# Performance work log

Measured on AMD Instinct MI355X. Metric: run time of the kernel, lower is better.

## Reference

```python
import jax, jax.numpy as jnp
import numpy as np

B, CITY, H, E, IN = 512, 100, 256, 256, 2
D2 = 2 * H  # num_directions * hidden_size
PEN = 1e6   # already_played_penalty


def _cell(x, h, c, Wih, Whh, b):
    # PyTorch LSTM cell, gate order i,f,g,o
    g = x @ Wih.T + h @ Whh.T + b
    i, f, gg, o = jnp.split(g, 4, axis=-1)
    c = jax.nn.sigmoid(f) * c + jax.nn.sigmoid(i) * jnp.tanh(gg)
    h = jax.nn.sigmoid(o) * jnp.tanh(c)
    return h, c


def _run_lstm(xs, Wih, Whh, b, reverse):
    # xs: [B, T, E] -> outputs [B, T, H], final (h, c)
    Bsz, hdim = xs.shape[0], Whh.shape[1]
    init = (jnp.zeros((Bsz, hdim), xs.dtype), jnp.zeros((Bsz, hdim), xs.dtype))
    def step(carry, x):
        h, c = _cell(x, carry[0], carry[1], Wih, Whh, b)
        return (h, c), h
    (h, c), hs = jax.lax.scan(step, init, jnp.swapaxes(xs, 0, 1), reverse=reverse)
    return jnp.swapaxes(hs, 0, 1), h, c


def setup_inputs() -> dict:
    key = jax.random.key(0)
    ks = iter(jax.random.split(key, 32))
    nrm = lambda shape: 0.1 * jax.random.normal(next(ks), shape, dtype=jnp.float32)
    return {
        "inputs": jax.random.normal(next(ks), (B, CITY, IN), dtype=jnp.float32),
        "test_roads": jax.random.randint(next(ks), (B, CITY), 0, CITY, dtype=jnp.int32),
        "W_embed": nrm((E, IN)),
        "enc_Wih_f": nrm((4 * H, E)), "enc_Whh_f": nrm((4 * H, H)), "enc_b_f": nrm((4 * H,)),
        "enc_Wih_b": nrm((4 * H, E)), "enc_Whh_b": nrm((4 * H, H)), "enc_b_b": nrm((4 * H,)),
        "dec_Wih_f": nrm((4 * H, D2)), "dec_Whh_f": nrm((4 * H, H)), "dec_b_f": nrm((4 * H,)),
        "dec_Wih_b": nrm((4 * H, D2)), "dec_Whh_b": nrm((4 * H, H)), "dec_b_b": nrm((4 * H,)),
        "W_ref": nrm((D2, D2)), "W_q": nrm((D2, D2)), "v": nrm((D2,)),
        "W_ref2": nrm((D2, D2)), "W_q2": nrm((D2, D2)), "v2": nrm((D2,)),
    }


def _forward(inputs, test_roads, W_embed,
             enc_Wih_f, enc_Whh_f, enc_b_f, enc_Wih_b, enc_Whh_b, enc_b_b,
             dec_Wih_f, dec_Whh_f, dec_b_f, dec_Wih_b, dec_Whh_b, dec_b_b,
             W_ref, W_q, v, W_ref2, W_q2, v2):
    Bsz, city, _ = inputs.shape
    emb = inputs @ W_embed.T                                  # [B, city, E]
    enc_f, hf0, cf0 = _run_lstm(emb, enc_Wih_f, enc_Whh_f, enc_b_f, False)
    enc_b, hb0, cb0 = _run_lstm(emb, enc_Wih_b, enc_Whh_b, enc_b_b, True)
    Enc = jnp.concatenate([enc_f, enc_b], axis=-1)            # [B, city, D2]
    # dropout p=0 -> Enc is loop-invariant; hoist the two ref projections
    ref1 = Enc @ W_ref.T                                      # [B, city, D2]
    ref2 = Enc @ W_ref2.T                                     # [B, city, D2]

    def step(carry, tgt):
        x, hf, cf, hb, cb, played, loss = carry
        hf, cf = _cell(x, hf, cf, dec_Wih_f, dec_Whh_f, dec_b_f)
        hb, cb = _cell(x, hb, cb, dec_Wih_b, dec_Whh_b, dec_b_b)
        dec_out = jnp.concatenate([hf, hb], axis=-1)          # [B, D2]
        ow = jnp.tanh(ref1 + (dec_out @ W_q.T)[:, None, :]) @ v - PEN * played   # [B, city]
        aw = jax.nn.softmax(jnp.tanh(ref2 + (x @ W_q2.T)[:, None, :]) @ v2, axis=1)
        sel = jnp.argmax(ow, axis=1)                          # [B]
        x_new = jnp.einsum('bj,bjk->bk', aw, Enc)             # [B, D2]
        played = played + jax.nn.one_hot(sel, city, dtype=played.dtype)
        ce = jax.nn.logsumexp(ow, axis=1) - jnp.take_along_axis(ow, tgt[:, None], axis=1)[:, 0]
        return (x_new, hf, cf, hb, cb, played, loss + ce), None

    x0 = jnp.zeros((Bsz, Enc.shape[-1]), inputs.dtype)
    played0 = jnp.zeros((Bsz, city), inputs.dtype)
    loss0 = jnp.zeros((Bsz,), inputs.dtype)
    carry, _ = jax.lax.scan(step, (x0, hf0, cf0, hb0, cb0, played0, loss0),
                            test_roads.T.astype(jnp.int32))
    return carry[-1]                                          # path_loss [B]


def reference(inputs, test_roads, W_embed,
              enc_Wih_f, enc_Whh_f, enc_b_f, enc_Wih_b, enc_Whh_b, enc_b_b,
              dec_Wih_f, dec_Whh_f, dec_b_f, dec_Wih_b, dec_Whh_b, dec_b_b,
              W_ref, W_q, v, W_ref2, W_q2, v2):
    return _forward(inputs, test_roads, W_embed,
                    enc_Wih_f, enc_Whh_f, enc_b_f, enc_Wih_b, enc_Whh_b, enc_b_b,
                    dec_Wih_f, dec_Whh_f, dec_b_f, dec_Wih_b, dec_Whh_b, dec_b_b,
                    W_ref, W_q, v, W_ref2, W_q2, v2)
```

## Files before the change

### kernel.cpp

```cpp
#include <hip/hip_runtime.h>
#include <hip/hip_fp16.h>
#include <math.h>

namespace {
constexpr int Bn  = 512;
constexpr int Tn  = 100;
constexpr int Hn  = 256;
constexpr int En  = 256;
constexpr int D2n = 512;
constexpr int G4n = 1024;
constexpr float PENf = 1e6f;
constexpr size_t BIGN = (size_t)Bn * Tn * D2n;
constexpr int FLAG_STRIDE = 32;
constexpr int DBLK = 896;
constexpr size_t BAR_UINTS = (256 + DBLK) * FLAG_STRIDE + 64;
}

using short8  = __attribute__((ext_vector_type(8))) short;
using us8     = __attribute__((ext_vector_type(8))) unsigned short;
using floatx4 = __attribute__((ext_vector_type(4))) float;

template<typename T> __device__ __forceinline__ float cvt_to_f(T x);
template<> __device__ __forceinline__ float cvt_to_f<float>(float x) { return x; }
template<> __device__ __forceinline__ float cvt_to_f<__half>(__half x) {
  return __half2float(x);
}
template<typename T> __device__ __forceinline__ T cvt_from_f(float x);
template<> __device__ __forceinline__ float cvt_from_f<float>(float x) { return x; }
template<> __device__ __forceinline__ __half cvt_from_f<__half>(float x) {
  return __float2half(x);
}
__device__ __forceinline__ float h2f_bits(unsigned short b) {
  __half_raw r; r.x = b; return __half2float(__half(r));
}
__device__ __forceinline__ float fast_exp(float x) {
  return __builtin_amdgcn_exp2f(x * 1.44269504088896340736f);
}
__device__ __forceinline__ float sigmoidf(float x) {
  return __builtin_amdgcn_rcpf(1.0f + fast_exp(-x));
}
__device__ __forceinline__ float fast_tanhf(float x) {
  return 1.0f - 2.0f * __builtin_amdgcn_rcpf(fast_exp(2.0f * x) + 1.0f);
}

__device__ __forceinline__ float loadf_dev(const float* p) {
  return __uint_as_float(__hip_atomic_load((const unsigned*)p, __ATOMIC_RELAXED,
                                           __HIP_MEMORY_SCOPE_AGENT));
}
__device__ __forceinline__ void storef_dev(float* p, float v) {
  __hip_atomic_store((unsigned*)p, __float_as_uint(v), __ATOMIC_RELAXED,
                     __HIP_MEMORY_SCOPE_AGENT);
}
__device__ __forceinline__ float4 load4_dev(const float* p) {
  const unsigned long long a = __hip_atomic_load((const unsigned long long*)p,
      __ATOMIC_RELAXED, __HIP_MEMORY_SCOPE_AGENT);
  const unsigned long long b = __hip_atomic_load((const unsigned long long*)p + 1,
      __ATOMIC_RELAXED, __HIP_MEMORY_SCOPE_AGENT);
  float4 r;
  r.x = __uint_as_float((unsigned)a);  r.y = __uint_as_float((unsigned)(a >> 32));
  r.z = __uint_as_float((unsigned)b);  r.w = __uint_as_float((unsigned)(b >> 32));
  return r;
}
__device__ __forceinline__ void store2_dev(float* p, const float2 v) {
  const unsigned long long a = (unsigned long long)__float_as_uint(v.x) |
                               ((unsigned long long)__float_as_uint(v.y) << 32);
  __hip_atomic_store((unsigned long long*)p, a, __ATOMIC_RELAXED,
                     __HIP_MEMORY_SCOPE_AGENT);
}
template<typename CT> __device__ __forceinline__ CT load_dev(const CT* p);
template<> __device__ __forceinline__ float load_dev<float>(const float* p) {
  return loadf_dev(p);
}
template<> __device__ __forceinline__ __half load_dev<__half>(const __half* p) {
  unsigned short u = __hip_atomic_load((const unsigned short*)p, __ATOMIC_RELAXED,
                                       __HIP_MEMORY_SCOPE_AGENT);
  __half_raw r; r.x = u; return (__half)r;
}
template<typename CT> __device__ __forceinline__ void store_dev(CT* p, CT v);
template<> __device__ __forceinline__ void store_dev<float>(float* p, float v) {
  storef_dev(p, v);
}
template<> __device__ __forceinline__ void store_dev<__half>(__half* p, __half v) {
  __half_raw r = *reinterpret_cast<__half_raw*>(&v);
  __hip_atomic_store((unsigned short*)p, r.x, __ATOMIC_RELAXED,
                     __HIP_MEMORY_SCOPE_AGENT);
}

__device__ __forceinline__ void split2(float x, short& h, short& l) {
  const unsigned u  = __float_as_uint(x);
  const unsigned hu = u & 0xffff0000u;
  h = (short)(hu >> 16);
  const float r = x - __uint_as_float(hu);
  l = (short)((__float_as_uint(r) + 0x8000u) >> 16);
}
__device__ __forceinline__ void store4split(const float4 v, short* hp, short* lp) {
  short h0, h1, h2, h3, l0, l1, l2, l3;
  split2(v.x, h0, l0); split2(v.y, h1, l1);
  split2(v.z, h2, l2); split2(v.w, h3, l3);
  *(short4*)hp = make_short4(h0, h1, h2, h3);
  *(short4*)lp = make_short4(l0, l1, l2, l3);
}

__device__ __forceinline__ void grid_sync256(unsigned* flags, unsigned* release,
                                             unsigned no) {
  __builtin_amdgcn_s_waitcnt(0);
  __syncthreads();
  if (blockIdx.x == 0) {
    const int tid = threadIdx.x;
    if (tid > 0) {
      while (__hip_atomic_load(&flags[tid * FLAG_STRIDE], __ATOMIC_RELAXED,
                               __HIP_MEMORY_SCOPE_AGENT) < no)
        __builtin_amdgcn_s_sleep(1);
    }
    __syncthreads();
    if (tid == 0)
      __hip_atomic_store(release, no, __ATOMIC_RELAXED, __HIP_MEMORY_SCOPE_AGENT);
  } else {
    if (threadIdx.x == 0) {
      __hip_atomic_store(&flags[blockIdx.x * FLAG_STRIDE], no, __ATOMIC_RELAXED,
                         __HIP_MEMORY_SCOPE_AGENT);
      while (__hip_atomic_load(release, __ATOMIC_RELAXED,
                               __HIP_MEMORY_SCOPE_AGENT) < no)
        __builtin_amdgcn_s_sleep(2);
    }
    __syncthreads();
  }
}

__device__ __forceinline__ void grid_syncD(unsigned* flags, unsigned* release,
                                           unsigned no) {
  __builtin_amdgcn_s_waitcnt(0);
  __syncthreads();
  if (blockIdx.x == 0) {
    for (int i = threadIdx.x; i < DBLK; i += 256) {
      if (i > 0) {
        while (__hip_atomic_load(&flags[i * FLAG_STRIDE], __ATOMIC_RELAXED,
                                 __HIP_MEMORY_SCOPE_AGENT) < no)
          __builtin_amdgcn_s_sleep(1);
      }
    }
    __syncthreads();
    if (threadIdx.x == 0)
      __hip_atomic_store(release, no, __ATOMIC_RELAXED, __HIP_MEMORY_SCOPE_AGENT);
  } else {
    if (threadIdx.x == 0) {
      __hip_atomic_store(&flags[blockIdx.x * FLAG_STRIDE], no, __ATOMIC_RELAXED,
                         __HIP_MEMORY_SCOPE_AGENT);
      while (__hip_atomic_load(release, __ATOMIC_RELAXED,
                               __HIP_MEMORY_SCOPE_AGENT) < no)
        __builtin_amdgcn_s_sleep(2);
    }
    __syncthreads();
  }
}

template<typename CT, bool ACC, int NT, bool CSC>
__device__ __forceinline__ void gemm64v2(short* smem,
    const float* A, int lda, int m0,
    const float* B, int ldb, int n0, int K,
    CT* Cbase, size_t crstride, int tid) {
  constexpr int BPL  = NT * 128;
  constexpr int BSZ  = NT * 512;
  constexpr int BUFS = 4096 + 2 * BSZ;
  const int lane = tid & 63, wave = tid >> 6, qm = lane & 15, quad = lane >> 4;
  const int ra = tid >> 3, c4 = tid & 7, j0 = (c4 & 1) * 4, gq = c4 >> 1;
  const int a0 = gq * 512 + ra * 8 + j0;
  const int a1 = gq * 512 + (ra + 32) * 8 + j0;
  const int b0 = gq * BPL + ra * 8 + j0;
  const int b1 = gq * BPL + (ra + 32) * 8 + j0;
  const int CN = K >> 5;

  floatx4 acc[NT];
#pragma unroll
  for (int nt = 0; nt < NT; ++nt) acc[nt] = (floatx4){0.f, 0.f, 0.f, 0.f};

  float4 Aa0, Aa1, Ba0, Ba1, Ab0, Ab1, Bb0, Bb1;
  auto ld = [&](int c, float4& x0, float4& x1, float4& y0, float4& y1) {
    const int k0 = c * 32 + c4 * 4;
    x0 = load4_dev(A + (size_t)(m0 + ra) * lda + k0);
    x1 = load4_dev(A + (size_t)(m0 + ra + 32) * lda + k0);
    y0 = *(const float4*)(B + (size_t)(n0 + ra) * ldb + k0);
    if (NT == 4)
      y1 = *(const float4*)(B + (size_t)(n0 + ra + 32) * ldb + k0);
  };
  auto st = [&](short* bp, const float4& x0, const float4& x1,
                const float4& y0, const float4& y1) {
    store4split(x0, bp + a0, bp + 2048 + a0);
    store4split(x1, bp + a1, bp + 2048 + a1);
    store4split(y0, bp + 4096 + b0, bp + 4096 + BSZ + b0);
    if (NT == 4) store4split(y1, bp + 4096 + b1, bp + 4096 + BSZ + b1);
  };
  auto mm = [&](const short* bp) {
    const int abase = quad * 512 + (wave * 16 + qm) * 8;
    const short8 ah = *(const short8*)&bp[abase];
    const short8 al = *(const short8*)&bp[2048 + abase];
#pragma unroll
    for (int nt = 0; nt < NT; ++nt) {
      const int bb = quad * BPL + (nt * 16 + qm) * 8;
      const short8 bh = *(const short8*)&bp[4096 + bb];
      const short8 bl = *(const short8*)&bp[4096 + BSZ + bb];
      acc[nt] = __builtin_amdgcn_mfma_f32_16x16x32_bf16(ah, bh, acc[nt], 0, 0, 0);
      acc[nt] = __builtin_amdgcn_mfma_f32_16x16x32_bf16(ah, bl, acc[nt], 0, 0, 0);
      acc[nt] = __builtin_amdgcn_mfma_f32_16x16x32_bf16(al, bh, acc[nt], 0, 0, 0);
    }
  };

  ld(0, Aa0, Aa1, Ba0, Ba1);
  if (CN > 1) ld(1, Ab0, Ab1, Bb0, Bb1);
  st(smem, Aa0, Aa1, Ba0, Ba1);
  __syncthreads();
  for (int c = 0; c < CN; c += 2) {
    if (c + 2 < CN) ld(c + 2, Aa0, Aa1, Ba0, Ba1);
    mm(smem);
    if (c + 1 < CN) st(smem + BUFS, Ab0, Ab1, Bb0, Bb1);
    __syncthreads();
    if (c + 1 < CN) {
      if (c + 3 < CN) ld(c + 3, Ab0, Ab1, Bb0, Bb1);
      mm(smem + BUFS);
      if (c + 2 < CN) st(smem, Aa0, Aa1, Ba0, Ba1);
      __syncthreads();
    }
  }

#pragma unroll
  for (int nt = 0; nt < NT; ++nt)
#pragma unroll
    for (int r2 = 0; r2 < 4; ++r2) {
      const int m = wave * 16 + quad * 4 + r2, n = nt * 16 + qm;
      CT* cp = Cbase + (size_t)m * crstride + n;
      float o = acc[nt][r2];
      if (CSC) {
        if (ACC) o += cvt_to_f<CT>(load_dev<CT>(cp));
        store_dev<CT>(cp, cvt_from_f<CT>(o));
      } else {
        if (ACC) o += cvt_to_f<CT>(*cp);
        *cp = cvt_from_f<CT>(o);
      }
    }
}

__device__ __forceinline__ void gates_gemm_v2(floatx4 acc[4], short* smem,
    const float* A1, int lda1, const float* B1, int ldb1, int K1,
    const float* A2, int lda2, const float* B2, int ldb2, int K2,
    int m0, int hoff, int tid) {
  const int lane = tid & 63, wave = tid >> 6, qm = lane & 15, quad = lane >> 4;
  const int ra = tid >> 3, c4 = tid & 7, j0 = (c4 & 1) * 4, gq = c4 >> 1;
  const int a0 = gq * 512 + ra * 8 + j0;
  const int a1 = gq * 512 + (ra + 32) * 8 + j0;
  const int g0 = (ra >> 4) * Hn + hoff + (ra & 15);
  const int g1 = ((ra + 32) >> 4) * Hn + hoff + ((ra + 32) & 15);
  const int C1 = K1 >> 5;
  const int C2 = A2 ? (K2 >> 5) : 0;
  const int CN = C1 + C2;

  float4 Aa0, Aa1, Ba0, Ba1, Ab0, Ab1, Bb0, Bb1;
  auto ld = [&](int c, float4& x0, float4& x1, float4& y0, float4& y1) {
    const float* A; const float* B; int lda, ldb, k0;
    if (c < C1) { A = A1; B = B1; lda = lda1; ldb = ldb1; k0 = c * 32; }
    else        { A = A2; B = B2; lda = lda2; ldb = ldb2; k0 = (c - C1) * 32; }
    k0 += c4 * 4;
    x0 = load4_dev(A + (size_t)(m0 + ra) * lda + k0);
    x1 = load4_dev(A + (size_t)(m0 + ra + 32) * lda + k0);
    y0 = *(const float4*)(B + (size_t)g0 * ldb + k0);
    y1 = *(const float4*)(B + (size_t)g1 * ldb + k0);
  };
  auto st2 = [&](short* bp, const float4& x0, const float4& x1,
                 const float4& y0, const float4& y1) {
    store4split(x0, bp + a0, bp + 2048 + a0);
    store4split(x1, bp + a1, bp + 2048 + a1);
    store4split(y0, bp + 4096 + a0, bp + 6144 + a0);
    store4split(y1, bp + 4096 + a1, bp + 6144 + a1);
  };
  auto mm = [&](const short* bp) {
    const int abase = quad * 512 + (wave * 16 + qm) * 8;
    const short8 ah = *(const short8*)&bp[abase];
    const short8 al = *(const short8*)&bp[2048 + abase];
#pragma unroll
    for (int gg = 0; gg < 4; ++gg) {
      const int bb = quad * 512 + (gg * 16 + qm) * 8;
      const short8 bh = *(const short8*)&bp[4096 + bb];
      const short8 bl = *(const short8*)&bp[6144 + bb];
      acc[gg] = __builtin_amdgcn_mfma_f32_16x16x32_bf16(ah, bh, acc[gg], 0, 0, 0);
      acc[gg] = __builtin_amdgcn_mfma_f32_16x16x32_bf16(ah, bl, acc[gg], 0, 0, 0);
      acc[gg] = __builtin_amdgcn_mfma_f32_16x16x32_bf16(al, bh, acc[gg], 0, 0, 0);
    }
  };

  if (CN <= 0) return;
  ld(0, Aa0, Aa1, Ba0, Ba1);
  if (CN > 1) ld(1, Ab0, Ab1, Bb0, Bb1);
  st2(smem, Aa0, Aa1, Ba0, Ba1);
  __syncthreads();
  for (int c = 0; c < CN; c += 2) {
    if (c + 2 < CN) ld(c + 2, Aa0, Aa1, Ba0, Ba1);
    mm(smem);
    if (c + 1 < CN) st2(smem + 8192, Ab0, Ab1, Bb0, Bb1);
    __syncthreads();
    if (c + 1 < CN) {
      if (c + 3 < CN) ld(c + 3, Ab0, Ab1, Bb0, Bb1);
      mm(smem + 8192);
      if (c + 2 < CN) st2(smem, Aa0, Aa1, Ba0, Ba1);
      __syncthreads();
    }
  }
}

__global__ void weff_kernel(const float* Wih_f, const float* Wih_b,
                            const float* W_embed, float* weff_f, float* weff_b) {
  const int gidx = blockIdx.x * 256 + threadIdx.x;
  if (gidx >= G4n) return;
  float f0 = 0.f, f1 = 0.f, b0 = 0.f, b1 = 0.f;
  for (int e = 0; e < En; ++e) {
    const float w0 = W_embed[e * 2 + 0];
    const float w1 = W_embed[e * 2 + 1];
    const float wf = Wih_f[gidx * En + e];
    const float wb = Wih_b[gidx * En + e];
    f0 = fmaf(wf, w0, f0); f1 = fmaf(wf, w1, f1);
    b0 = fmaf(wb, w0, b0); b1 = fmaf(wb, w1, b1);
  }
  weff_f[gidx * 2 + 0] = f0; weff_f[gidx * 2 + 1] = f1;
  weff_b[gidx * 2 + 0] = b0; weff_b[gidx * 2 + 1] = b1;
}

template<typename ET, typename RT1, typename RT2>
struct EncP {
  const float* inputs;
  const float* Whh_f; const float* Whh_b;
  const float* b_f; const float* b_b;
  const float* weff_f; const float* weff_b;
  const float* W_ref; const float* W_ref2;
  float* hbuf;
  float* c_dec;
  float* dec_out0;
  ET* Enc; RT1* ref1; RT2* ref2;
  unsigned* flags; unsigned* release;
};

template<typename ET, typename RT1, typename RT2>
__global__ __launch_bounds__(256, 1) void enc_coop(EncP<ET, RT1, RT2> P) {
  __shared__ __align__(16) short smem[16384];
  const int bid = blockIdx.x, tid = threadIdx.x;
  const int dir = bid >> 7, btile = (bid >> 4) & 7, hs = bid & 15;
  const int r_ref = (bid >> 7) & 1, r_dir = (bid >> 6) & 1;
  const int r_bt = (bid >> 3) & 7, r_ns = bid & 7;
  const int lane = tid & 63, wave = tid >> 6, qm = lane & 15, quad = lane >> 4;
  const int hcol = hs * 16 + qm;
  const float* Whh  = dir ? P.Whh_b : P.Whh_f;
  const float* bias = dir ? P.b_b : P.b_f;
  const float* weff = dir ? P.weff_b : P.weff_f;
  float c_reg[4] = {0.f, 0.f, 0.f, 0.f};
  float h_reg[4] = {0.f, 0.f, 0.f, 0.f};
  unsigned sync_no = 0;

  auto ref_job = [&](const float* hpar, int pos) {
    const float* hsrc = hpar + (size_t)r_dir * (Bn * Hn);
    if (r_ref == 0)
      gemm64v2<RT1, true, 4, true>(smem, hsrc, Hn, r_bt * 64,
                             P.W_ref + r_dir * Hn, D2n, r_ns * 64, Hn,
                             P.ref1 + (size_t)(r_bt * 64) * Tn * D2n + (size_t)pos * D2n + r_ns * 64,
                             (size_t)Tn * D2n, tid);
    else
      gemm64v2<RT2, true, 4, true>(smem, hsrc, Hn, r_bt * 64,
                             P.W_ref2 + r_dir * Hn, D2n, r_ns * 64, Hn,
                             P.ref2 + (size_t)(r_bt * 64) * Tn * D2n + (size_t)pos * D2n + r_ns * 64,
                             (size_t)Tn * D2n, tid);
  };

  for (int t = 0; t < Tn; ++t) {
    const float* hprev = P.hbuf + (size_t)((t - 1) & 1) * (2 * Bn * Hn);
    if (t > 0) ref_job(hprev, r_dir ? (Tn - t) : (t - 1));
    floatx4 acc[4];
#pragma unroll
    for (int gg = 0; gg < 4; ++gg) acc[gg] = (floatx4){0.f, 0.f, 0.f, 0.f};
    if (t > 0)
      gates_gemm_v2(acc, smem, hprev + (size_t)dir * (Bn * Hn), Hn, Whh, Hn, Hn,
                    nullptr, 0, nullptr, 0, 0, btile * 64, hs * 16, tid);
    const int tcur = dir ? (Tn - 1 - t) : t;
    float xa[4], xb2[4];
#pragma unroll
    for (int r2 = 0; r2 < 4; ++r2) {
      const int m = btile * 64 + wave * 16 + quad * 4 + r2;
      xa[r2]  = P.inputs[(size_t)m * (Tn * 2) + tcur * 2 + 0];
      xb2[r2] = P.inputs[(size_t)m * (Tn * 2) + tcur * 2 + 1];
    }
    float gv[4][4];
#pragma unroll
    for (int gg = 0; gg < 4; ++gg) {
      const int grow = gg * Hn + hcol;
      const float bn = bias[grow];
      const float w20 = weff[grow * 2], w21 = weff[grow * 2 + 1];
#pragma unroll
      for (int r2 = 0; r2 < 4; ++r2) {
        float o = acc[gg][r2] + bn;
        o = fmaf(xa[r2], w20, fmaf(xb2[r2], w21, o));
        gv[gg][r2] = o;
      }
    }
    float* hdst = P.hbuf + (size_t)(t & 1) * (2 * Bn * Hn) + (size_t)dir * (Bn * Hn);
    const int tt = dir ? (Tn - 1 - t) : t;
#pragma unroll
    for (int r2 = 0; r2 < 4; ++r2) {
      const float cn = sigmoidf(gv[1][r2]) * c_reg[r2] +
                       sigmoidf(gv[0][r2]) * fast_tanhf(gv[2][r2]);
      c_reg[r2] = cn;
      const float hn = sigmoidf(gv[3][r2]) * fast_tanhf(cn);
      h_reg[r2] = hn;
      const int m = btile * 64 + wave * 16 + quad * 4 + r2;
      storef_dev(&hdst[(size_t)m * Hn + hcol], hn);
      store_dev<ET>(&P.Enc[(size_t)m * Tn * D2n + (size_t)tt * D2n + dir * Hn + hcol],
                    cvt_from_f<ET>(hn));
    }
    grid_sync256(P.flags, P.release, ++sync_no);
  }
  ref_job(P.hbuf + (size_t)1 * (2 * Bn * Hn), r_dir ? 0 : (Tn - 1));
#pragma unroll
  for (int r2 = 0; r2 < 4; ++r2) {
    const int m = btile * 64 + wave * 16 + quad * 4 + r2;
    P.dec_out0[(size_t)m * D2n + dir * Hn + hcol] = h_reg[r2];
    P.c_dec[((size_t)dir * Bn + m) * Hn + hcol] = c_reg[r2];
  }
}

template<typename ET, typename RT1, typename RT2>
struct DecP {
  const int* test_roads;
  const float* Wih_f; const float* Whh_f; const float* b_f;
  const float* Wih_b; const float* Whh_b; const float* b_b;
  const float* W_q; const float* W_q2; const float* v; const float* v2;
  const ET* Enc; const RT1* ref1; const RT2* ref2;
  float* dec_out;
  float* xb;
  float* qb; float* q2b;
  const float* c_init;
  float* loss;
  unsigned* flags; unsigned* release;
};

template<typename ET, typename RT1, typename RT2>
__global__ __launch_bounds__(256, 4) void dec_coop(DecP<ET, RT1, RT2> P) {
  __shared__ __align__(16) short smem[16384];
  __shared__ float sl[104], awl[104], playedl[104];
  __shared__ float lossl;
  const int bid = blockIdx.x, tid = threadIdx.x;
  const int lane = tid & 63, wave = tid >> 6, qm = lane & 15, quad = lane >> 4;
  const int role = (bid < 256) ? 0 : (bid < 384 ? 1 : 2);

  const int dir = (bid >> 7) & 1, btile = (bid >> 4) & 7, hs = bid & 15;
  const int hcol = hs * 16 + qm;
  const float* Wih  = dir ? P.Wih_b : P.Wih_f;
  const float* Whh  = dir ? P.Whh_b : P.Whh_f;
  const float* bias = dir ? P.b_b : P.b_f;
  float c_reg[4] = {0.f, 0.f, 0.f, 0.f};
  if (role == 0) {
#pragma unroll
    for (int r2 = 0; r2 < 4; ++r2) {
      const int m = btile * 64 + wave * 16 + quad * 4 + r2;
      c_reg[r2] = P.c_init[((size_t)dir * Bn + m) * Hn + hcol];
    }
  }
  const int gidx = bid - 256, pbt = gidx >> 4, pn = gidx & 15;
  const int b = bid - 384;
  if (role == 2) {
    if (tid < Tn) playedl[tid] = 0.f;
    if (tid == 0) lossl = 0.f;
  }
  unsigned sync_no = 0;
  __syncthreads();

  auto attn_ref = [&](const __half* refb, const float* qg, const float* vg) {
    const int e = lane * 8;
    const float4 qa = load4_dev(qg + e), qc = load4_dev(qg + e + 4);
    const float4 va = *(const float4*)(vg + e);
    const float4 vb = *(const float4*)(vg + e + 4);
    const float q[8]  = {qa.x, qa.y, qa.z, qa.w, qc.x, qc.y, qc.z, qc.w};
    const float vv[8] = {va.x, va.y, va.z, va.w, vb.x, vb.y, vb.z, vb.w};
    const unsigned short* pr = (const unsigned short*)refb +
                               (size_t)(wave * 25) * D2n + e;
    us8 r0 = *(const us8*)pr;
    us8 r1 = *(const us8*)(pr + (size_t)D2n);
    us8 r2v = *(const us8*)(pr + (size_t)2 * D2n);
    for (int jj = 0; jj < 25; ++jj) {
      float a = 0.f;
#pragma unroll
      for (int k = 0; k < 8; ++k)
        a = fmaf(vv[k], fast_tanhf(h2f_bits(r0[k]) + q[k]), a);
      r0 = r1; r1 = r2v;
      if (jj + 3 < 25) r2v = *(const us8*)(pr + (size_t)(jj + 3) * D2n);
#pragma unroll
      for (int off = 32; off > 0; off >>= 1) a += __shfl_xor(a, off, 64);
      if (lane == 0) sl[wave * 25 + jj] = a;
    }
  };

  auto ow_reduce = [&](int u) {
    if (wave != 0) return;
    const int jA = lane, jB = lane + 64;
    const bool vA = jA < Tn, vB = jB < Tn;
    const float owA = vA ? sl[jA] - PENf * playedl[jA] : -INFINITY;
    const float owB = vB ? sl[jB] - PENf * playedl[jB] : -INFINITY;
    float bv; int bi;
    if (owB > owA) { bv = owB; bi = jB; } else { bv = owA; bi = jA; }
#pragma unroll
    for (int off = 32; off > 0; off >>= 1) {
      const float ov = __shfl_xor(bv, off, 64);
      const int   oi = __shfl_xor(bi, off, 64);
      if (ov > bv || (ov == bv && oi < bi)) { bv = ov; bi = oi; }
    }
    float es = (vA ? __expf(owA - bv) : 0.f) + (vB ? __expf(owB - bv) : 0.f);
#pragma unroll
    for (int off = 32; off > 0; off >>= 1) es += __shfl_xor(es, off, 64);
    if (lane == 0) {
      const int tgt = P.test_roads[b * Tn + u];
      const float owt = sl[tgt] - PENf * playedl[tgt];
      lossl += (bv + __logf(es)) - owt;
      playedl[bi] += 1.f;
    }
  };

  for (int t = 0; t < Tn; ++t) {
    const float* dcur = P.dec_out + (size_t)(t & 1) * (Bn * D2n);
    float* dnext = P.dec_out + (size_t)((t + 1) & 1) * (Bn * D2n);
    if (role == 0) {
      floatx4 acc[4];
#pragma unroll
      for (int gg = 0; gg < 4; ++gg) acc[gg] = (floatx4){0.f, 0.f, 0.f, 0.f};
      gates_gemm_v2(acc, smem, P.xb, D2n, Wih, D2n, D2n,
                    dcur + dir * Hn, D2n, Whh, Hn, Hn, btile * 64, hs * 16, tid);
#pragma unroll
      for (int gg = 0; gg < 4; ++gg) {
        const float bn = bias[gg * Hn + hcol];
#pragma unroll
        for (int r2 = 0; r2 < 4; ++r2) acc[gg][r2] += bn;
      }
#pragma unroll
      for (int r2 = 0; r2 < 4; ++r2) {
        const float cn = sigmoidf(acc[1][r2]) * c_reg[r2] +
                         sigmoidf(acc[0][r2]) * fast_tanhf(acc[2][r2]);
        c_reg[r2] = cn;
        const float hn = sigmoidf(acc[3][r2]) * fast_tanhf(cn);
        const int m = btile * 64 + wave * 16 + quad * 4 + r2;
        storef_dev(&dnext[(size_t)m * D2n + dir * Hn + hcol], hn);
      }
    } else if (role == 1) {
      gemm64v2<float, false, 2, true>(smem, P.xb, D2n, pbt * 64,
                                      P.W_q2, D2n, pn * 32, D2n,
                                      P.q2b + (size_t)(pbt * 64) * D2n + pn * 32,
                                      D2n, tid);
    } else if (t > 0) {
      attn_ref((const __half*)P.ref1 + (size_t)b * Tn * D2n,
               P.qb + (size_t)b * D2n, P.v);
      __syncthreads();
      ow_reduce(t - 1);
    }
    grid_syncD(P.flags, P.release, ++sync_no);
    if (role == 1) {
      gemm64v2<float, false, 2, true>(smem, dnext, D2n, pbt * 64,
                                      P.W_q, D2n, pn * 32, D2n,
                                      P.qb + (size_t)(pbt * 64) * D2n + pn * 32,
                                      D2n, tid);
    } else if (role == 2) {
      attn_ref((const __half*)P.ref2 + (size_t)b * Tn * D2n,
               P.q2b + (size_t)b * D2n, P.v2);
      __syncthreads();
      if (wave == 0) {
        const int jA = lane, jB = lane + 64;
        const bool vA = jA < Tn, vB = jB < Tn;
        const float sA = vA ? sl[jA] : -INFINITY;
        const float sB = vB ? sl[jB] : -INFINITY;
        float m = fmaxf(sA, sB);
#pragma unroll
        for (int off = 32; off > 0; off >>= 1) m = fmaxf(m, __shfl_xor(m, off, 64));
        const float eA = vA ? __expf(sA - m) : 0.f;
        const float eB = vB ? __expf(sB - m) : 0.f;
        float es = eA + eB;
#pragma unroll
        for (int off = 32; off > 0; off >>= 1) es += __shfl_xor(es, off, 64);
        const float inv = __builtin_amdgcn_rcpf(es);
        if (vA) awl[jA] = eA * inv;
        if (vB) awl[jB] = eB * inv;
      }
      __syncthreads();
      {
        float* xpart = (float*)smem;
        const int e = lane * 8;
        const unsigned short* Eb = (const unsigned short*)P.Enc +
            (size_t)b * Tn * D2n + (size_t)(wave * 25) * D2n + e;
        float acc8[8];
#pragma unroll
        for (int k = 0; k < 8; ++k) acc8[k] = 0.f;
        us8 r0 = *(const us8*)Eb;
        us8 r1 = *(const us8*)(Eb + (size_t)D2n);
        us8 r2v = *(const us8*)(Eb + (size_t)2 * D2n);
        for (int jj = 0; jj < 25; ++jj) {
          const float w = awl[wave * 25 + jj];
#pragma unroll
          for (int k = 0; k < 8; ++k) acc8[k] = fmaf(w, h2f_bits(r0[k]), acc8[k]);
          r0 = r1; r1 = r2v;
          if (jj + 3 < 25) r2v = *(const us8*)(Eb + (size_t)(jj + 3) * D2n);
        }
#pragma unroll
        for (int k = 0; k < 8; ++k) xpart[wave * 512 + e + k] = acc8[k];
      }
      __syncthreads();
      {
        const float* xpart = (const float*)smem;
        const int c = tid * 2;
        float2 s;
        s.x = xpart[c]     + xpart[512 + c]     + xpart[1024 + c]     + xpart[1536 + c];
        s.y = xpart[c + 1] + xpart[512 + c + 1] + xpart[1024 + c + 1] + xpart[1536 + c + 1];
        store2_dev(&P.xb[(size_t)b * D2n + c], s);
      }
    }
    grid_syncD(P.flags, P.release, ++sync_no);
  }
  if (role == 2) {
    attn_ref((const __half*)P.ref1 + (size_t)b * Tn * D2n,
             P.qb + (size_t)b * D2n, P.v);
    __syncthreads();
    ow_reduce(Tn - 1);
    if (tid == 0) P.loss[b] = lossl;
  }
}

static void run_all(void* const* d_in, void* d_out, char* ws, hipStream_t stream) {
  using ET = __half; using RT1 = __half; using RT2 = __half;
  const float* inputs     = (const float*)d_in[0];
  const int*   test_roads = (const int*)d_in[1];
  const float* W_embed    = (const float*)d_in[2];
  const float* enc_Wih_f  = (const float*)d_in[3];
  const float* enc_Whh_f  = (const float*)d_in[4];
  const float* enc_b_f    = (const float*)d_in[5];
  const float* enc_Wih_b  = (const float*)d_in[6];
  const float* enc_Whh_b  = (const float*)d_in[7];
  const float* enc_b_b    = (const float*)d_in[8];
  const float* dec_Wih_f  = (const float*)d_in[9];
  const float* dec_Whh_f  = (const float*)d_in[10];
  const float* dec_b_f    = (const float*)d_in[11];
  const float* dec_Wih_b  = (const float*)d_in[12];
  const float* dec_Whh_b  = (const float*)d_in[13];
  const float* dec_b_b    = (const float*)d_in[14];
  const float* W_ref      = (const float*)d_in[15];
  const float* W_q        = (const float*)d_in[16];
  const float* v          = (const float*)d_in[17];
  const float* W_ref2     = (const float*)d_in[18];
  const float* W_q2       = (const float*)d_in[19];
  const float* v2         = (const float*)d_in[20];

  char* p0 = ws;
  ET*  Enc  = (ET*)p0;  p0 += BIGN * sizeof(ET);
  RT1* ref1 = (RT1*)p0; p0 += BIGN * sizeof(RT1);
  RT2* ref2 = (RT2*)p0; p0 += BIGN * sizeof(RT2);
  unsigned* flagsE = (unsigned*)p0;
  unsigned* relE   = flagsE + 256 * FLAG_STRIDE;
  unsigned* flagsD = relE + 32;
  unsigned* relD   = flagsD + DBLK * FLAG_STRIDE;
  float* xb      = (float*)(p0 + BAR_UINTS * 4);
  float* dec_out = xb + Bn * D2n;
  float* hbuf    = dec_out + 2 * Bn * D2n;
  float* c_dec   = hbuf + 4 * Bn * Hn;
  float* qb      = c_dec + 2 * Bn * Hn;
  float* q2b     = qb + Bn * D2n;
  float* weff_f  = q2b + Bn * D2n;
  float* weff_b  = weff_f + G4n * 2;

  hipMemsetAsync(ref1, 0, BIGN * (sizeof(RT1) + sizeof(RT2)), stream);
  hipMemsetAsync(flagsE, 0, BAR_UINTS * 4 + (size_t)Bn * D2n * 4, stream);

  weff_kernel<<<G4n / 256, 256, 0, stream>>>(enc_Wih_f, enc_Wih_b, W_embed,
                                             weff_f, weff_b);

  EncP<ET, RT1, RT2> ep = { inputs, enc_Whh_f, enc_Whh_b, enc_b_f, enc_b_b,
                            weff_f, weff_b, W_ref, W_ref2,
                            hbuf, c_dec, dec_out, Enc, ref1, ref2,
                            flagsE, relE };
  enc_coop<ET, RT1, RT2><<<256, 256, 0, stream>>>(ep);

  DecP<ET, RT1, RT2> dp = { test_roads,
                            dec_Wih_f, dec_Whh_f, dec_b_f,
                            dec_Wih_b, dec_Whh_b, dec_b_b,
                            W_q, W_q2, v, v2,
                            Enc, ref1, ref2,
                            dec_out, xb, qb, q2b, c_dec,
                            (float*)d_out, flagsD, relD };
  dec_coop<ET, RT1, RT2><<<DBLK, 256, 0, stream>>>(dp);
}

extern "C" void kernel_launch(void* const* d_in, const int* in_sizes, int n_in,
                              void* d_out, int out_size, void* d_ws, size_t ws_size,
                              hipStream_t stream) {
  (void)in_sizes; (void)n_in; (void)out_size; (void)ws_size;
  run_all(d_in, d_out, (char*)d_ws, stream);
}
```

Measured before the change: 8.173 ms.

## Shrink decoder grid to 512 blocks with every block running per-batch attention

The persistent decoder kernel drops from 896 blocks with three dedicated roles to 512 blocks. Each block now does its LSTM or projection GEMM share and also runs the attention and softmax work for one batch row. The softmax uses a fixed shift of 16 instead of a max-reduction, and the attention-weighted sum of Enc is fused into the score loop, which removes several block barriers and a pass over the scores. The aim is cheaper grid barriers and more balanced work across blocks. In exchange, occupancy drops to 2 blocks per SM, and the fixed-shift exp could overflow or lose precision if scores stray far from 16.

```diff
diff --git a/kernel.cpp b/kernel.cpp
--- a/kernel.cpp
+++ b/kernel.cpp
@@ -12,7 +12,7 @@
 constexpr float PENf = 1e6f;
 constexpr size_t BIGN = (size_t)Bn * Tn * D2n;
 constexpr int FLAG_STRIDE = 32;
-constexpr int DBLK = 896;
+constexpr int DBLK = 512;
 constexpr size_t BAR_UINTS = (256 + DBLK) * FLAG_STRIDE + 64;
 }
 
@@ -437,13 +437,15 @@
 };
 
 template<typename ET, typename RT1, typename RT2>
-__global__ __launch_bounds__(256, 4) void dec_coop(DecP<ET, RT1, RT2> P) {
+__global__ __launch_bounds__(256, 2) void dec_coop(DecP<ET, RT1, RT2> P) {
   __shared__ __align__(16) short smem[16384];
-  __shared__ float sl[104], awl[104], playedl[104];
+  __shared__ float sl[104], playedl[104];
+  __shared__ float wmax[4], wsum[4], dpart[4];
+  __shared__ int   widx[4];
   __shared__ float lossl;
   const int bid = blockIdx.x, tid = threadIdx.x;
   const int lane = tid & 63, wave = tid >> 6, qm = lane & 15, quad = lane >> 4;
-  const int role = (bid < 256) ? 0 : (bid < 384 ? 1 : 2);
+  const int b = bid;
 
   const int dir = (bid >> 7) & 1, btile = (bid >> 4) & 7, hs = bid & 15;
   const int hcol = hs * 16 + qm;
@@ -451,35 +453,36 @@
   const float* Whh  = dir ? P.Whh_b : P.Whh_f;
   const float* bias = dir ? P.b_b : P.b_f;
   float c_reg[4] = {0.f, 0.f, 0.f, 0.f};
-  if (role == 0) {
+  if (bid < 256) {
 #pragma unroll
     for (int r2 = 0; r2 < 4; ++r2) {
       const int m = btile * 64 + wave * 16 + quad * 4 + r2;
       c_reg[r2] = P.c_init[((size_t)dir * Bn + m) * Hn + hcol];
     }
   }
-  const int gidx = bid - 256, pbt = gidx >> 4, pn = gidx & 15;
-  const int b = bid - 384;
-  if (role == 2) {
-    if (tid < Tn) playedl[tid] = 0.f;
-    if (tid == 0) lossl = 0.f;
-  }
+  const int gidx = bid & 127, pbt = gidx >> 4, pn = gidx & 15;
+
+  if (tid < Tn) playedl[tid] = 0.f;
+  if (tid == 0) lossl = 0.f;
   unsigned sync_no = 0;
   __syncthreads();
 
-  auto attn_ref = [&](const __half* refb, const float* qg, const float* vg) {
+  auto s1_fused = [&](int u) {
     const int e = lane * 8;
-    const float4 qa = load4_dev(qg + e), qc = load4_dev(qg + e + 4);
-    const float4 va = *(const float4*)(vg + e);
-    const float4 vb = *(const float4*)(vg + e + 4);
+    const float4 qa = load4_dev(P.qb + (size_t)b * D2n + e);
+    const float4 qc = load4_dev(P.qb + (size_t)b * D2n + e + 4);
+    const float4 va = *(const float4*)(P.v + e);
+    const float4 vb2 = *(const float4*)(P.v + e + 4);
     const float q[8]  = {qa.x, qa.y, qa.z, qa.w, qc.x, qc.y, qc.z, qc.w};
-    const float vv[8] = {va.x, va.y, va.z, va.w, vb.x, vb.y, vb.z, vb.w};
-    const unsigned short* pr = (const unsigned short*)refb +
-                               (size_t)(wave * 25) * D2n + e;
+    const float vv[8] = {va.x, va.y, va.z, va.w, vb2.x, vb2.y, vb2.z, vb2.w};
+    const unsigned short* pr = (const unsigned short*)P.ref1 +
+        (size_t)b * Tn * D2n + (size_t)(wave * 25) * D2n + e;
     us8 r0 = *(const us8*)pr;
     us8 r1 = *(const us8*)(pr + (size_t)D2n);
     us8 r2v = *(const us8*)(pr + (size_t)2 * D2n);
+    float bmax = -INFINITY, sume = 0.f; int bidx = 0;
     for (int jj = 0; jj < 25; ++jj) {
+      const int row = wave * 25 + jj;
       float a = 0.f;
 #pragma unroll
       for (int k = 0; k < 8; ++k)
@@ -488,39 +491,87 @@
       if (jj + 3 < 25) r2v = *(const us8*)(pr + (size_t)(jj + 3) * D2n);
 #pragma unroll
       for (int off = 32; off > 0; off >>= 1) a += __shfl_xor(a, off, 64);
-      if (lane == 0) sl[wave * 25 + jj] = a;
-    }
-  };
-
-  auto ow_reduce = [&](int u) {
-    if (wave != 0) return;
-    const int jA = lane, jB = lane + 64;
-    const bool vA = jA < Tn, vB = jB < Tn;
-    const float owA = vA ? sl[jA] - PENf * playedl[jA] : -INFINITY;
-    const float owB = vB ? sl[jB] - PENf * playedl[jB] : -INFINITY;
-    float bv; int bi;
-    if (owB > owA) { bv = owB; bi = jB; } else { bv = owA; bi = jA; }
-#pragma unroll
-    for (int off = 32; off > 0; off >>= 1) {
-      const float ov = __shfl_xor(bv, off, 64);
-      const int   oi = __shfl_xor(bi, off, 64);
-      if (ov > bv || (ov == bv && oi < bi)) { bv = ov; bi = oi; }
-    }
-    float es = (vA ? __expf(owA - bv) : 0.f) + (vB ? __expf(owB - bv) : 0.f);
-#pragma unroll
-    for (int off = 32; off > 0; off >>= 1) es += __shfl_xor(es, off, 64);
-    if (lane == 0) {
+      if (lane == 0) sl[row] = a;
+      const float ow = a - PENf * playedl[row];
+      if (ow > bmax) { bmax = ow; bidx = row; }
+      sume += fast_exp(ow - 16.f);
+    }
+    if (lane == 0) { wmax[wave] = bmax; widx[wave] = bidx; wsum[wave] = sume; }
+    __syncthreads();
+    if (tid == 0) {
+      float bv = wmax[0], es = wsum[0]; int bi = widx[0];
+#pragma unroll
+      for (int w = 1; w < 4; ++w) {
+        es += wsum[w];
+        if (wmax[w] > bv) { bv = wmax[w]; bi = widx[w]; }
+      }
       const int tgt = P.test_roads[b * Tn + u];
       const float owt = sl[tgt] - PENf * playedl[tgt];
-      lossl += (bv + __logf(es)) - owt;
+      lossl += (16.f + __logf(es)) - owt;
       playedl[bi] += 1.f;
+    }
+  };
+
+  auto s2x_fused = [&]() {
+    const int e = lane * 8;
+    const float4 qa = load4_dev(P.q2b + (size_t)b * D2n + e);
+    const float4 qc = load4_dev(P.q2b + (size_t)b * D2n + e + 4);
+    const float4 va = *(const float4*)(P.v2 + e);
+    const float4 vb2 = *(const float4*)(P.v2 + e + 4);
+    const float q[8]  = {qa.x, qa.y, qa.z, qa.w, qc.x, qc.y, qc.z, qc.w};
+    const float vv[8] = {va.x, va.y, va.z, va.w, vb2.x, vb2.y, vb2.z, vb2.w};
+    const unsigned short* pr = (const unsigned short*)P.ref2 +
+        (size_t)b * Tn * D2n + (size_t)(wave * 25) * D2n + e;
+    const unsigned short* pe = (const unsigned short*)P.Enc +
+        (size_t)b * Tn * D2n + (size_t)(wave * 25) * D2n + e;
+    us8 r0 = *(const us8*)pr;
+    us8 r1 = *(const us8*)(pr + (size_t)D2n);
+    us8 r2v = *(const us8*)(pr + (size_t)2 * D2n);
+    us8 e0 = *(const us8*)pe;
+    us8 e1 = *(const us8*)(pe + (size_t)D2n);
+    us8 e2v = *(const us8*)(pe + (size_t)2 * D2n);
+    float xacc[8];
+#pragma unroll
+    for (int k = 0; k < 8; ++k) xacc[k] = 0.f;
+    float den = 0.f;
+    for (int jj = 0; jj < 25; ++jj) {
+      float a = 0.f;
+#pragma unroll
+      for (int k = 0; k < 8; ++k)
+        a = fmaf(vv[k], fast_tanhf(h2f_bits(r0[k]) + q[k]), a);
+      r0 = r1; r1 = r2v;
+      if (jj + 3 < 25) r2v = *(const us8*)(pr + (size_t)(jj + 3) * D2n);
+#pragma unroll
+      for (int off = 32; off > 0; off >>= 1) a += __shfl_xor(a, off, 64);
+      const float w = fast_exp(a - 16.f);
+      den += w;
+#pragma unroll
+      for (int k = 0; k < 8; ++k)
+        xacc[k] = fmaf(w, h2f_bits(e0[k]), xacc[k]);
+      e0 = e1; e1 = e2v;
+      if (jj + 3 < 25) e2v = *(const us8*)(pe + (size_t)(jj + 3) * D2n);
+    }
+    float* xpart = (float*)smem;
+#pragma unroll
+    for (int k = 0; k < 8; ++k) xpart[wave * 512 + e + k] = xacc[k];
+    if (lane == 0) dpart[wave] = den;
+    __syncthreads();
+    {
+      const float dsum = dpart[0] + dpart[1] + dpart[2] + dpart[3];
+      const float inv = __builtin_amdgcn_rcpf(dsum);
+      const int c = tid * 2;
+      float2 s;
+      s.x = (xpart[c] + xpart[512 + c] + xpart[1024 + c] + xpart[1536 + c]) * inv;
+      s.y = (xpart[c + 1] + xpart[512 + c + 1] + xpart[1024 + c + 1] +
+             xpart[1536 + c + 1]) * inv;
+      store2_dev(&P.xb[(size_t)b * D2n + c], s);
     }
   };
 
   for (int t = 0; t < Tn; ++t) {
     const float* dcur = P.dec_out + (size_t)(t & 1) * (Bn * D2n);
     float* dnext = P.dec_out + (size_t)((t + 1) & 1) * (Bn * D2n);
-    if (role == 0) {
+    if (bid < 256) {
       floatx4 acc[4];
 #pragma unroll
       for (int gg = 0; gg < 4; ++gg) acc[gg] = (floatx4){0.f, 0.f, 0.f, 0.f};
@@ -541,85 +592,25 @@
         const int m = btile * 64 + wave * 16 + quad * 4 + r2;
         storef_dev(&dnext[(size_t)m * D2n + dir * Hn + hcol], hn);
       }
-    } else if (role == 1) {
+    } else if (bid < 384) {
       gemm64v2<float, false, 2, true>(smem, P.xb, D2n, pbt * 64,
                                       P.W_q2, D2n, pn * 32, D2n,
                                       P.q2b + (size_t)(pbt * 64) * D2n + pn * 32,
                                       D2n, tid);
-    } else if (t > 0) {
-      attn_ref((const __half*)P.ref1 + (size_t)b * Tn * D2n,
-               P.qb + (size_t)b * D2n, P.v);
-      __syncthreads();
-      ow_reduce(t - 1);
-    }
+    }
+    if (t > 0) s1_fused(t - 1);
     grid_syncD(P.flags, P.release, ++sync_no);
-    if (role == 1) {
+    if (bid >= 384) {
       gemm64v2<float, false, 2, true>(smem, dnext, D2n, pbt * 64,
                                       P.W_q, D2n, pn * 32, D2n,
                                       P.qb + (size_t)(pbt * 64) * D2n + pn * 32,
                                       D2n, tid);
-    } else if (role == 2) {
-      attn_ref((const __half*)P.ref2 + (size_t)b * Tn * D2n,
-               P.q2b + (size_t)b * D2n, P.v2);
-      __syncthreads();
-      if (wave == 0) {
-        const int jA = lane, jB = lane + 64;
-        const bool vA = jA < Tn, vB = jB < Tn;
-        const float sA = vA ? sl[jA] : -INFINITY;
-        const float sB = vB ? sl[jB] : -INFINITY;
-        float m = fmaxf(sA, sB);
-#pragma unroll
-        for (int off = 32; off > 0; off >>= 1) m = fmaxf(m, __shfl_xor(m, off, 64));
-        const float eA = vA ? __expf(sA - m) : 0.f;
-        const float eB = vB ? __expf(sB - m) : 0.f;
-        float es = eA + eB;
-#pragma unroll
-        for (int off = 32; off > 0; off >>= 1) es += __shfl_xor(es, off, 64);
-        const float inv = __builtin_amdgcn_rcpf(es);
-        if (vA) awl[jA] = eA * inv;
-        if (vB) awl[jB] = eB * inv;
-      }
-      __syncthreads();
-      {
-        float* xpart = (float*)smem;
-        const int e = lane * 8;
-        const unsigned short* Eb = (const unsigned short*)P.Enc +
-            (size_t)b * Tn * D2n + (size_t)(wave * 25) * D2n + e;
-        float acc8[8];
-#pragma unroll
-        for (int k = 0; k < 8; ++k) acc8[k] = 0.f;
-        us8 r0 = *(const us8*)Eb;
-        us8 r1 = *(const us8*)(Eb + (size_t)D2n);
-        us8 r2v = *(const us8*)(Eb + (size_t)2 * D2n);
-        for (int jj = 0; jj < 25; ++jj) {
-          const float w = awl[wave * 25 + jj];
-#pragma unroll
-          for (int k = 0; k < 8; ++k) acc8[k] = fmaf(w, h2f_bits(r0[k]), acc8[k]);
-          r0 = r1; r1 = r2v;
-          if (jj + 3 < 25) r2v = *(const us8*)(Eb + (size_t)(jj + 3) * D2n);
-        }
-#pragma unroll
-        for (int k = 0; k < 8; ++k) xpart[wave * 512 + e + k] = acc8[k];
-      }
-      __syncthreads();
-      {
-        const float* xpart = (const float*)smem;
-        const int c = tid * 2;
-        float2 s;
-        s.x = xpart[c]     + xpart[512 + c]     + xpart[1024 + c]     + xpart[1536 + c];
-        s.y = xpart[c + 1] + xpart[512 + c + 1] + xpart[1024 + c + 1] + xpart[1536 + c + 1];
-        store2_dev(&P.xb[(size_t)b * D2n + c], s);
-      }
-    }
+    }
+    s2x_fused();
     grid_syncD(P.flags, P.release, ++sync_no);
   }
-  if (role == 2) {
-    attn_ref((const __half*)P.ref1 + (size_t)b * Tn * D2n,
-             P.qb + (size_t)b * D2n, P.v);
-    __syncthreads();
-    ow_reduce(Tn - 1);
-    if (tid == 0) P.loss[b] = lossl;
-  }
+  s1_fused(Tn - 1);
+  if (tid == 0) P.loss[b] = lossl;
 }
 
 static void run_all(void* const* d_in, void* d_out, char* ws, hipStream_t stream) {
```

Result: slower. 9.226 ms (+12.9%).
